# Optimization experiments

Hardware: AMD Instinct MI355X
Metric: run time of the kernel (lower is better)

## Reference

```python
import jax, jax.numpy as jnp
import numpy as np

K = 10          # number of neighbors (init kwarg k)
NUM_CLASSES = 100  # label vocabulary (targets drawn in [0, 100))


def setup_inputs() -> dict:
    key = jax.random.key(0)
    k1, k2, k3 = jax.random.split(key, 3)
    X = jax.random.normal(k1, (1024, 512), dtype=jnp.float32)
    data = jax.random.normal(k2, (50000, 512), dtype=jnp.float32)
    targets = jax.random.randint(k3, (50000,), 0, NUM_CLASSES, dtype=jnp.int64)
    return {"X": X, "data": data, "targets": targets}


def reference(X, data, targets):
    # Pairwise L2 distance (p=2 path of the module), computed via the
    x2 = jnp.sum(X * X, axis=1, keepdims=True)              # [Q, 1]
    d2 = jnp.sum(data * data, axis=1)                        # [N]
    sq = x2 + d2[None, :] - 2.0 * (X @ data.T)               # [Q, N]
    dist = jnp.sqrt(jnp.maximum(sq, 0.0))                    # torch.norm(p1-p2, p=2)

    # torch: sort distances ascending, take first k indices -> top-k smallest.
    _, idx = jax.lax.top_k(-dist, K)                         # [Q, K]
    labels = targets[idx]                                    # [Q, K]

    # torch.mode over the k neighbor labels: histogram + argmax.
    # argmax picks the first (smallest) class on ties, matching torch.mode.
    counts = jax.nn.one_hot(labels, NUM_CLASSES, dtype=jnp.float32).sum(axis=1)  # [Q, C]
    pred = jnp.argmax(counts, axis=1).astype(jnp.float32)    # [Q]
    return pred
```

## Files before the change

kernel.cpp:

```cpp
#include <hip/hip_runtime.h>
#include <math.h>
#include <limits.h>

#define QN 1024
#define NN 50000
#define NPAD 50048
#define DD 512
#define KNN 10
#define NT 128
#define QTB 128
#define BK 32
#define NS 391
#define QB 8
#define NSAMP 31
#define NREST (NS - NSAMP)
#define CAP 512

#define WS_D2  0
#define WS_TAU 50048
#define WS_CNT (WS_TAU + 2048)
#define WS_XH  (WS_CNT + 1024)
#define WS_XL  (WS_XH + QN * DD / 2)
#define WS_CKS (WS_XL + QN * DD / 2)
#define WS_BUF (WS_CKS + QN * NSAMP * KNN * 2)
#define WS_DH  (WS_BUF + QN * CAP * 2)
#define WS_DL  (WS_DH + NS * 16 * 2048)
#define WS_END (WS_DL + NS * 16 * 2048)

typedef __attribute__((ext_vector_type(8))) short short8;
typedef __attribute__((ext_vector_type(4))) float f32x4;
typedef unsigned long long u64;

__device__ __forceinline__ u64 mkkey(float f, int idx) {
  unsigned u = __float_as_uint(f);
  unsigned m = u ^ ((unsigned)((int)u >> 31) | 0x80000000u);
  return ((u64)m << 32) | (unsigned)idx;
}

__device__ __forceinline__ void cvt2(float x, float y, unsigned& hi, unsigned& lo) {
  unsigned ux = __float_as_uint(x), uy = __float_as_uint(y);
  unsigned rx = ux + 0x7fffu + ((ux >> 16) & 1u);
  unsigned ry = uy + 0x7fffu + ((uy >> 16) & 1u);
  hi = (rx >> 16) | (ry & 0xffff0000u);
  float xl = x - __uint_as_float(rx & 0xffff0000u);
  float yl = y - __uint_as_float(ry & 0xffff0000u);
  unsigned uxl = __float_as_uint(xl), uyl = __float_as_uint(yl);
  unsigned rxl = uxl + 0x7fffu + ((uxl >> 16) & 1u);
  unsigned ryl = uyl + 0x7fffu + ((uyl >> 16) & 1u);
  lo = (rxl >> 16) | (ryl & 0xffff0000u);
}

__device__ __forceinline__ void glds16(const void* g, void* l) {
  __builtin_amdgcn_global_load_lds(
      (const __attribute__((address_space(1))) unsigned*)g,
      (__attribute__((address_space(3))) unsigned*)l, 16, 0, 0);
}

__device__ __forceinline__ void ins10(u64* kl, u64 k) {
#pragma unroll
  for (int u = 0; u < KNN; u++) {
    u64 lo = (k < kl[u]) ? k : kl[u];
    u64 hi = (k < kl[u]) ? kl[u] : k;
    kl[u] = lo; k = hi;
  }
}

__global__ __launch_bounds__(256) void convx_kernel(
    const float* __restrict__ Xm, float* __restrict__ ws) {
  int w = threadIdx.x >> 6, lane = threadIdx.x & 63;
  int row = blockIdx.x * 4 + w;
  const float4* p = (const float4*)(Xm + (size_t)row * DD) + lane * 2;
  float4 v0 = p[0], v1 = p[1];
  unsigned h[4], l[4];
  cvt2(v0.x, v0.y, h[0], l[0]); cvt2(v0.z, v0.w, h[1], l[1]);
  cvt2(v1.x, v1.y, h[2], l[2]); cvt2(v1.z, v1.w, h[3], l[3]);
  ((uint4*)(ws + WS_XH))[row * 64 + lane] = make_uint4(h[0], h[1], h[2], h[3]);
  ((uint4*)(ws + WS_XL))[row * 64 + lane] = make_uint4(l[0], l[1], l[2], l[3]);
}

__global__ __launch_bounds__(256) void convd_kernel(
    const float* __restrict__ dat, float* __restrict__ ws) {
  const int slice = blockIdx.x;
  const int t = threadIdx.x;
  const int row = t >> 1, h2 = t & 1;
  const int gr = slice * NT + row;
  const int r15 = row & 15;
  float s = 0.f;
#pragma unroll
  for (int kc8 = 0; kc8 < 8; kc8++) {
    const int kc = h2 * 8 + kc8;
    float4 v[8];
    if (gr < NN) {
      const float4* src = (const float4*)(dat + (size_t)gr * DD + kc * 32);
#pragma unroll
      for (int j = 0; j < 8; j++) v[j] = src[j];
    } else {
#pragma unroll
      for (int j = 0; j < 8; j++) v[j] = make_float4(0.f, 0.f, 0.f, 0.f);
    }
    unsigned hw[16], lw[16];
#pragma unroll
    for (int j = 0; j < 8; j++) {
      s = fmaf(v[j].x, v[j].x, s); s = fmaf(v[j].y, v[j].y, s);
      s = fmaf(v[j].z, v[j].z, s); s = fmaf(v[j].w, v[j].w, s);
      cvt2(v[j].x, v[j].y, hw[2 * j], lw[2 * j]);
      cvt2(v[j].z, v[j].w, hw[2 * j + 1], lw[2 * j + 1]);
    }
    uint4* dhp = (uint4*)((unsigned char*)(ws + WS_DH) +
                          (((size_t)slice * 16 + kc) * 8 + (row >> 4)) * 1024);
    uint4* dlp = (uint4*)((unsigned char*)(ws + WS_DL) +
                          (((size_t)slice * 16 + kc) * 8 + (row >> 4)) * 1024);
#pragma unroll
    for (int qd = 0; qd < 4; qd++) {
      dhp[qd * 16 + r15] = make_uint4(hw[4 * qd], hw[4 * qd + 1], hw[4 * qd + 2], hw[4 * qd + 3]);
      dlp[qd * 16 + r15] = make_uint4(lw[4 * qd], lw[4 * qd + 1], lw[4 * qd + 2], lw[4 * qd + 3]);
    }
  }
  s += __shfl_xor(s, 1, 64);
  if (h2 == 0) ws[WS_D2 + gr] = (gr < NN) ? s : __builtin_inff();
}

struct StageT { unsigned char ah[8192], al[8192], bh[8192], bl[8192]; };
struct EpiT  { float sq[64][132]; };
struct ListT { u64 kl[64][4][KNN]; };
union SmemU { StageT s; EpiT e; ListT l; u64 tau[128]; };

template <int PRE, int MODE>
__global__ __launch_bounds__(256, 3) void knn_chunk(
    const float* __restrict__ dat, float* __restrict__ ws, int soff) {
  __shared__ __align__(16) SmemU sm;
  const int qbase = blockIdx.x * QTB;
  const int slice = blockIdx.y + soff;
  const int nbase = slice * NT;
  const int t = threadIdx.x;
  const int lane = t & 63, wave = t >> 6;
  const int wn = wave & 1, wq = wave >> 1;
  const unsigned short* xh = (const unsigned short*)(ws + WS_XH);
  const unsigned short* xl = (const unsigned short*)(ws + WS_XL);
  const unsigned char* dh = (const unsigned char*)(ws + WS_DH);
  const unsigned char* dl = (const unsigned char*)(ws + WS_DL);

  f32x4 acc[4][4];
#pragma unroll
  for (int i = 0; i < 4; i++)
#pragma unroll
    for (int j = 0; j < 4; j++) acc[i][j] = (f32x4)0.f;

  if (PRE) {
    auto stage = [&](int kc) {
#pragma unroll
      for (int i = 0; i < 4; i++) {
        int pp = wave * 4 + i;
        int p = pp & 7;
        const unsigned short* g = (pp < 8 ? xh : xl) +
            (size_t)(qbase + p * 16 + (lane & 15)) * DD + kc * 32 + (lane >> 4) * 8;
        glds16(g, (pp < 8 ? sm.s.ah : sm.s.al) + p * 1024);
      }
#pragma unroll
      for (int i = 0; i < 4; i++) {
        int pp = wave * 4 + i;
        int p = pp & 7;
        const unsigned char* g = (pp < 8 ? dh : dl) +
            (((size_t)slice * 16 + kc) * 8 + p) * 1024 + lane * 16;
        glds16(g, (pp < 8 ? sm.s.bh : sm.s.bl) + p * 1024);
      }
    };
    stage(0);
    for (int kc = 0; kc < 16; kc++) {
      __syncthreads();
      const int fragoff = lane * 16;
      short8 fah[4], fal[4], fbh[4], fbl[4];
#pragma unroll
      for (int i = 0; i < 4; i++) {
        fah[i] = *(const short8*)(sm.s.ah + (wq * 4 + i) * 1024 + fragoff);
        fal[i] = *(const short8*)(sm.s.al + (wq * 4 + i) * 1024 + fragoff);
        fbh[i] = *(const short8*)(sm.s.bh + (wn * 4 + i) * 1024 + fragoff);
        fbl[i] = *(const short8*)(sm.s.bl + (wn * 4 + i) * 1024 + fragoff);
      }
      __syncthreads();
      if (kc < 15) stage(kc + 1);
#pragma unroll
      for (int mt = 0; mt < 4; mt++)
#pragma unroll
        for (int nt = 0; nt < 4; nt++)
          acc[mt][nt] = __builtin_amdgcn_mfma_f32_16x16x32_bf16(fah[mt], fbh[nt], acc[mt][nt], 0, 0, 0);
#pragma unroll
      for (int mt = 0; mt < 4; mt++)
#pragma unroll
        for (int nt = 0; nt < 4; nt++)
          acc[mt][nt] = __builtin_amdgcn_mfma_f32_16x16x32_bf16(fah[mt], fbl[nt], acc[mt][nt], 0, 0, 0);
#pragma unroll
      for (int mt = 0; mt < 4; mt++)
#pragma unroll
        for (int nt = 0; nt < 4; nt++)
          acc[mt][nt] = __builtin_amdgcn_mfma_f32_16x16x32_bf16(fal[mt], fbh[nt], acc[mt][nt], 0, 0, 0);
    }
  } else {
    const int brow = t >> 1, bh_half = t & 1;
    const int bgr = nbase + brow;
    const int bpanel = (brow >> 4) * 1024;
    const int bchunk = (brow & 15) * 16;
    for (int kk = 0; kk < DD; kk += BK) {
      __syncthreads();
#pragma unroll
      for (int i = 0; i < 4; i++) {
        int pp = wave * 4 + i;
        int p = pp & 7;
        const unsigned short* g = (pp < 8 ? xh : xl) +
            (size_t)(qbase + p * 16 + (lane & 15)) * DD + kk + (lane >> 4) * 8;
        glds16(g, (pp < 8 ? sm.s.ah : sm.s.al) + p * 1024);
      }
      {
        float4 v0 = make_float4(0.f, 0.f, 0.f, 0.f), v1 = v0, v2 = v0, v3 = v0;
        if (bgr < NN) {
          const float4* src = (const float4*)(dat + (size_t)bgr * DD + kk + bh_half * 16);
          v0 = src[0]; v1 = src[1]; v2 = src[2]; v3 = src[3];
        }
        unsigned hw[8], lw[8];
        cvt2(v0.x, v0.y, hw[0], lw[0]); cvt2(v0.z, v0.w, hw[1], lw[1]);
        cvt2(v1.x, v1.y, hw[2], lw[2]); cvt2(v1.z, v1.w, hw[3], lw[3]);
        cvt2(v2.x, v2.y, hw[4], lw[4]); cvt2(v2.z, v2.w, hw[5], lw[5]);
        cvt2(v3.x, v3.y, hw[6], lw[6]); cvt2(v3.z, v3.w, hw[7], lw[7]);
        unsigned char* bhp = sm.s.bh + bpanel;
        unsigned char* blp = sm.s.bl + bpanel;
        *(uint4*)(bhp + (2 * bh_half) * 256 + bchunk)     = make_uint4(hw[0], hw[1], hw[2], hw[3]);
        *(uint4*)(bhp + (2 * bh_half + 1) * 256 + bchunk) = make_uint4(hw[4], hw[5], hw[6], hw[7]);
        *(uint4*)(blp + (2 * bh_half) * 256 + bchunk)     = make_uint4(lw[0], lw[1], lw[2], lw[3]);
        *(uint4*)(blp + (2 * bh_half + 1) * 256 + bchunk) = make_uint4(lw[4], lw[5], lw[6], lw[7]);
      }
      __syncthreads();
      const int fragoff = lane * 16;
      short8 fah[4], fal[4], fbh[4], fbl[4];
#pragma unroll
      for (int i = 0; i < 4; i++) {
        fah[i] = *(const short8*)(sm.s.ah + (wq * 4 + i) * 1024 + fragoff);
        fal[i] = *(const short8*)(sm.s.al + (wq * 4 + i) * 1024 + fragoff);
        fbh[i] = *(const short8*)(sm.s.bh + (wn * 4 + i) * 1024 + fragoff);
        fbl[i] = *(const short8*)(sm.s.bl + (wn * 4 + i) * 1024 + fragoff);
      }
#pragma unroll
      for (int mt = 0; mt < 4; mt++)
#pragma unroll
        for (int nt = 0; nt < 4; nt++) {
          acc[mt][nt] = __builtin_amdgcn_mfma_f32_16x16x32_bf16(fah[mt], fbh[nt], acc[mt][nt], 0, 0, 0);
          acc[mt][nt] = __builtin_amdgcn_mfma_f32_16x16x32_bf16(fah[mt], fbl[nt], acc[mt][nt], 0, 0, 0);
          acc[mt][nt] = __builtin_amdgcn_mfma_f32_16x16x32_bf16(fal[mt], fbh[nt], acc[mt][nt], 0, 0, 0);
        }
    }
  }

  if (MODE == 0) {
#pragma unroll
    for (int pass = 0; pass < 2; pass++) {
      __syncthreads();
      if (wq == pass) {
#pragma unroll
        for (int nt = 0; nt < 4; nt++) {
          int col = wn * 64 + nt * 16 + (lane & 15);
          float d2v = ws[WS_D2 + nbase + col];
#pragma unroll
          for (int mt = 0; mt < 4; mt++)
#pragma unroll
            for (int rg = 0; rg < 4; rg++) {
              int lr = mt * 16 + (lane >> 4) * 4 + rg;
              sm.e.sq[lr][col] = fmaf(-2.f, acc[mt][nt][rg], d2v);
            }
        }
      }
      __syncthreads();
      {
        const int r = t >> 2, s = t & 3;
        u64 kl[KNN];
#pragma unroll
        for (int u = 0; u < KNN; u++) kl[u] = ~0ull;
        for (int jj = 0; jj < 32; jj++) {
          int c = s * 32 + ((jj + r + 8 * s) & 31);
          float v = sm.e.sq[r][c];
          ins10(kl, mkkey(v, nbase + c));
        }
        __syncthreads();
#pragma unroll
        for (int u = 0; u < KNN; u++) sm.l.kl[r][s][u] = kl[u];
      }
      __syncthreads();
      if (t < 64) {
        u64* dst = ((u64*)(ws + WS_CKS)) +
                   ((size_t)(qbase + pass * 64 + t) * NSAMP + blockIdx.y) * KNN;
        int h0 = 0, h1 = 0, h2 = 0, h3 = 0;
        for (int pick = 0; pick < KNN; pick++) {
          u64 k0 = sm.l.kl[t][0][h0], k1 = sm.l.kl[t][1][h1];
          u64 k2 = sm.l.kl[t][2][h2], k3 = sm.l.kl[t][3][h3];
          u64 best = k0; int bm = 0;
          if (k1 < best) { best = k1; bm = 1; }
          if (k2 < best) { best = k2; bm = 2; }
          if (k3 < best) { best = k3; bm = 3; }
          dst[pick] = best;
          h0 += (bm == 0); h1 += (bm == 1); h2 += (bm == 2); h3 += (bm == 3);
        }
      }
    }
  } else {
    __syncthreads();
    if (t < 128) sm.tau[t] = ((const u64*)(ws + WS_TAU))[qbase + t];
    __syncthreads();
    unsigned* cnt = (unsigned*)(ws + WS_CNT);
    u64* buf = (u64*)(ws + WS_BUF);
    float d2v[4];
#pragma unroll
    for (int nt = 0; nt < 4; nt++)
      d2v[nt] = ws[WS_D2 + nbase + wn * 64 + nt * 16 + (lane & 15)];
#pragma unroll
    for (int mt = 0; mt < 4; mt++)
#pragma unroll
      for (int rg = 0; rg < 4; rg++) {
        int row = wq * 64 + mt * 16 + (lane >> 4) * 4 + rg;
        u64 tr = sm.tau[row];
#pragma unroll
        for (int nt = 0; nt < 4; nt++) {
          float d = fmaf(-2.f, acc[mt][nt][rg], d2v[nt]);
          int col = nbase + wn * 64 + nt * 16 + (lane & 15);
          u64 key = mkkey(d, col);
          if (key < tr) {
            int q = qbase + row;
            unsigned slot = atomicAdd(cnt + q, 1u);
            if (slot < CAP) buf[(size_t)q * CAP + slot] = key;
          }
        }
      }
  }
}

__global__ __launch_bounds__(64) void tau_kernel(float* __restrict__ ws) {
  const int q = blockIdx.x;
  const int t = threadIdx.x;
  const u64* samp = ((const u64*)(ws + WS_CKS)) + (size_t)q * NSAMP * KNN;
  const int NC = NSAMP * KNN;
  u64 kl[KNN];
#pragma unroll
  for (int u = 0; u < KNN; u++) kl[u] = ~0ull;
  for (int j = t; j < NC; j += 64) ins10(kl, samp[j]);
  __shared__ u64 wk[64][KNN];
  __shared__ u64 m2[8][KNN];
#pragma unroll
  for (int u = 0; u < KNN; u++) wk[t][u] = kl[u];
  __syncthreads();
  if (t < 8) {
    int h[8] = {0, 0, 0, 0, 0, 0, 0, 0};
    for (int pick = 0; pick < KNN; pick++) {
      u64 best = ~0ull; int bm = 0;
#pragma unroll
      for (int m = 0; m < 8; m++) {
        u64 km = wk[t * 8 + m][h[m]];
        if (km < best) { best = km; bm = m; }
      }
      m2[t][pick] = best;
#pragma unroll
      for (int m = 0; m < 8; m++) h[m] += (bm == m);
    }
  }
  __syncthreads();
  if (t == 0) {
    int h[8] = {0, 0, 0, 0, 0, 0, 0, 0};
    u64 best = 0;
    for (int pick = 0; pick < KNN; pick++) {
      best = ~0ull; int bm = 0;
#pragma unroll
      for (int m = 0; m < 8; m++) {
        u64 km = m2[m][h[m]];
        if (km < best) { best = km; bm = m; }
      }
#pragma unroll
      for (int m = 0; m < 8; m++) h[m] += (bm == m);
    }
    ((u64*)(ws + WS_TAU))[q] = best;
    ((unsigned*)(ws + WS_CNT))[q] = 0u;
  }
}

__global__ __launch_bounds__(64) void knn_final(
    const int* __restrict__ targets, float* __restrict__ ws,
    float* __restrict__ out) {
  const int q = blockIdx.x;
  const int t = threadIdx.x;
  const u64* samp = ((const u64*)(ws + WS_CKS)) + (size_t)q * NSAMP * KNN;
  const u64* buf = ((const u64*)(ws + WS_BUF)) + (size_t)q * CAP;
  unsigned c = ((const unsigned*)(ws + WS_CNT))[q];
  if (c > CAP) c = CAP;

  u64 kl[KNN];
#pragma unroll
  for (int u = 0; u < KNN; u++) kl[u] = ~0ull;
  for (int j = t; j < NSAMP * KNN; j += 64) ins10(kl, samp[j]);
  for (int j = t; j < (int)c; j += 64) ins10(kl, buf[j]);

  __shared__ u64 wk[64][KNN];
  __shared__ u64 m2[8][KNN];
#pragma unroll
  for (int u = 0; u < KNN; u++) wk[t][u] = kl[u];
  __syncthreads();
  if (t < 8) {
    int h[8] = {0, 0, 0, 0, 0, 0, 0, 0};
    for (int pick = 0; pick < KNN; pick++) {
      u64 best = ~0ull; int bm = 0;
#pragma unroll
      for (int m = 0; m < 8; m++) {
        u64 km = wk[t * 8 + m][h[m]];
        if (km < best) { best = km; bm = m; }
      }
      m2[t][pick] = best;
#pragma unroll
      for (int m = 0; m < 8; m++) h[m] += (bm == m);
    }
  }
  __syncthreads();
  if (t == 0) {
    int h[8] = {0, 0, 0, 0, 0, 0, 0, 0};
    int fi[KNN];
    for (int pick = 0; pick < KNN; pick++) {
      u64 best = ~0ull; int bm = 0;
#pragma unroll
      for (int m = 0; m < 8; m++) {
        u64 km = m2[m][h[m]];
        if (km < best) { best = km; bm = m; }
      }
      fi[pick] = (int)(unsigned)(best & 0xffffffffu);
#pragma unroll
      for (int m = 0; m < 8; m++) h[m] += (bm == m);
    }
    int lab[KNN];
#pragma unroll
    for (int u = 0; u < KNN; u++) lab[u] = targets[fi[u]];
    int bc = 0, bl = INT_MAX;
#pragma unroll
    for (int i = 0; i < KNN; i++) {
      int cc = 0;
#pragma unroll
      for (int j = 0; j < KNN; j++) cc += (lab[j] == lab[i]) ? 1 : 0;
      if (cc > bc || (cc == bc && lab[i] < bl)) { bc = cc; bl = lab[i]; }
    }
    out[q] = (float)bl;
  }
}

extern "C" void kernel_launch(void* const* d_in, const int* in_sizes, int n_in,
                              void* d_out, int out_size, void* d_ws, size_t ws_size,
                              hipStream_t stream) {
  const float* Xm  = (const float*)d_in[0];
  const float* dat = (const float*)d_in[1];
  const int* targets = (const int*)d_in[2];
  float* out = (float*)d_out;
  float* ws  = (float*)d_ws;
  const bool pre = ws_size >= (size_t)WS_END * 4;

  hipLaunchKernelGGL(convx_kernel, dim3(QN / 4), dim3(256), 0, stream, Xm, ws);
  hipLaunchKernelGGL(convd_kernel, dim3(NS), dim3(256), 0, stream, dat, ws);
  if (pre) {
    hipLaunchKernelGGL((knn_chunk<1, 0>), dim3(QB, NSAMP), dim3(256), 0, stream, dat, ws, 0);
    hipLaunchKernelGGL(tau_kernel, dim3(QN), dim3(64), 0, stream, ws);
    hipLaunchKernelGGL((knn_chunk<1, 1>), dim3(QB, NREST), dim3(256), 0, stream, dat, ws, NSAMP);
  } else {
    hipLaunchKernelGGL((knn_chunk<0, 0>), dim3(QB, NSAMP), dim3(256), 0, stream, dat, ws, 0);
    hipLaunchKernelGGL(tau_kernel, dim3(QN), dim3(64), 0, stream, ws);
    hipLaunchKernelGGL((knn_chunk<0, 1>), dim3(QB, NREST), dim3(256), 0, stream, dat, ws, NSAMP);
  }
  hipLaunchKernelGGL(knn_final, dim3(QN), dim3(64), 0, stream, targets, ws, out);
}
```

Before: 387.4 us.

## Shrink MODE-1 shared memory, raise occupancy hint, and swizzle block order for L2 reuse

Specializes the shared-memory union per MODE, so the MODE-1 pass only reserves the 32 KB staging buffers instead of the larger epilogue and list arrays. It raises the launch-bounds minimum blocks per CU from 3 to 5. For MODE 1 it remaps block indices so that groups of eight consecutive blocks cover different data slices across query tiles, aiming for better L2 locality. The higher occupancy target may force the compiler to spill registers given the large 4x4 MFMA accumulator array, and it also applies to MODE 0, whose shared footprint is unchanged.

```diff
diff --git a/kernel.cpp b/kernel.cpp
--- a/kernel.cpp
+++ b/kernel.cpp
@@ -123,14 +123,26 @@
 struct StageT { unsigned char ah[8192], al[8192], bh[8192], bl[8192]; };
 struct EpiT  { float sq[64][132]; };
 struct ListT { u64 kl[64][4][KNN]; };
-union SmemU { StageT s; EpiT e; ListT l; u64 tau[128]; };
+
+template <int MODE> union SmemU { StageT s; EpiT e; ListT l; };
+template <> union SmemU<1> { StageT s; };
 
 template <int PRE, int MODE>
-__global__ __launch_bounds__(256, 3) void knn_chunk(
+__global__ __launch_bounds__(256, 5) void knn_chunk(
     const float* __restrict__ dat, float* __restrict__ ws, int soff) {
-  __shared__ __align__(16) SmemU sm;
-  const int qbase = blockIdx.x * QTB;
-  const int slice = blockIdx.y + soff;
+  __shared__ __align__(16) SmemU<MODE> sm;
+  int bqx, bsy;
+  if (MODE == 1 && (gridDim.y & 7) == 0) {
+    const int n = (int)(blockIdx.y * gridDim.x + blockIdx.x);
+    const int m = n >> 3;
+    const int ypx = (int)(gridDim.y >> 3);
+    bqx = m & 7;
+    bsy = (n & 7) * ypx + (m >> 3);
+  } else {
+    bqx = blockIdx.x; bsy = blockIdx.y;
+  }
+  const int qbase = bqx * QTB;
+  const int slice = bsy + soff;
   const int nbase = slice * NT;
   const int t = threadIdx.x;
   const int lane = t & 63, wave = t >> 6;
@@ -250,6 +262,7 @@
   }
 
   if (MODE == 0) {
+    SmemU<0>* smp = (SmemU<0>*)&sm;
 #pragma unroll
     for (int pass = 0; pass < 2; pass++) {
       __syncthreads();
@@ -263,7 +276,7 @@
 #pragma unroll
             for (int rg = 0; rg < 4; rg++) {
               int lr = mt * 16 + (lane >> 4) * 4 + rg;
-              sm.e.sq[lr][col] = fmaf(-2.f, acc[mt][nt][rg], d2v);
+              smp->e.sq[lr][col] = fmaf(-2.f, acc[mt][nt][rg], d2v);
             }
         }
       }
@@ -275,12 +288,12 @@
         for (int u = 0; u < KNN; u++) kl[u] = ~0ull;
         for (int jj = 0; jj < 32; jj++) {
           int c = s * 32 + ((jj + r + 8 * s) & 31);
-          float v = sm.e.sq[r][c];
+          float v = smp->e.sq[r][c];
           ins10(kl, mkkey(v, nbase + c));
         }
         __syncthreads();
 #pragma unroll
-        for (int u = 0; u < KNN; u++) sm.l.kl[r][s][u] = kl[u];
+        for (int u = 0; u < KNN; u++) smp->l.kl[r][s][u] = kl[u];
       }
       __syncthreads();
       if (t < 64) {
@@ -288,8 +301,8 @@
                    ((size_t)(qbase + pass * 64 + t) * NSAMP + blockIdx.y) * KNN;
         int h0 = 0, h1 = 0, h2 = 0, h3 = 0;
         for (int pick = 0; pick < KNN; pick++) {
-          u64 k0 = sm.l.kl[t][0][h0], k1 = sm.l.kl[t][1][h1];
-          u64 k2 = sm.l.kl[t][2][h2], k3 = sm.l.kl[t][3][h3];
+          u64 k0 = smp->l.kl[t][0][h0], k1 = smp->l.kl[t][1][h1];
+          u64 k2 = smp->l.kl[t][2][h2], k3 = smp->l.kl[t][3][h3];
           u64 best = k0; int bm = 0;
           if (k1 < best) { best = k1; bm = 1; }
           if (k2 < best) { best = k2; bm = 2; }
@@ -301,7 +314,8 @@
     }
   } else {
     __syncthreads();
-    if (t < 128) sm.tau[t] = ((const u64*)(ws + WS_TAU))[qbase + t];
+    u64* taub = (u64*)&sm;
+    if (t < 128) taub[t] = ((const u64*)(ws + WS_TAU))[qbase + t];
     __syncthreads();
     unsigned* cnt = (unsigned*)(ws + WS_CNT);
     u64* buf = (u64*)(ws + WS_BUF);
@@ -314,7 +328,7 @@
 #pragma unroll
       for (int rg = 0; rg < 4; rg++) {
         int row = wq * 64 + mt * 16 + (lane >> 4) * 4 + rg;
-        u64 tr = sm.tau[row];
+        u64 tr = taub[row];
 #pragma unroll
         for (int nt = 0; nt < 4; nt++) {
           float d = fmaf(-2.f, acc[mt][nt][rg], d2v[nt]);
```

New measurement: 735.3 us. +89.8%, slower.

## Pre-swizzle X into MFMA fragment layout and load A fragments directly from global

Applied to the files above, without the earlier changes.

convx now writes the bf16 hi/lo query matrix in MFMA fragment order, so the GEMM kernel loads A fragments straight from global/L2 into registers instead of staging them through LDS. That halves shared memory per block, which can raise occupancy, and removes the A-side LDS traffic. In return each wave issues more global loads. The MODE 1 kernel also remaps block indices so blocks that run together share query tiles across slices, aiming for better cache locality. Trade-off: A loads are no longer prefetched a stage ahead, so their latency may be exposed.

```diff
diff --git a/kernel.cpp b/kernel.cpp
--- a/kernel.cpp
+++ b/kernel.cpp
@@ -67,15 +67,17 @@
 
 __global__ __launch_bounds__(256) void convx_kernel(
     const float* __restrict__ Xm, float* __restrict__ ws) {
-  int w = threadIdx.x >> 6, lane = threadIdx.x & 63;
-  int row = blockIdx.x * 4 + w;
-  const float4* p = (const float4*)(Xm + (size_t)row * DD) + lane * 2;
+  const int g = blockIdx.x * 256 + threadIdx.x;
+  const int b = g >> 10, kc = (g >> 6) & 15, l = g & 63;
+  const int row = b * 16 + (l & 15);
+  const int col = kc * 32 + (l >> 4) * 8;
+  const float4* p = (const float4*)(Xm + (size_t)row * DD + col);
   float4 v0 = p[0], v1 = p[1];
-  unsigned h[4], l[4];
-  cvt2(v0.x, v0.y, h[0], l[0]); cvt2(v0.z, v0.w, h[1], l[1]);
-  cvt2(v1.x, v1.y, h[2], l[2]); cvt2(v1.z, v1.w, h[3], l[3]);
-  ((uint4*)(ws + WS_XH))[row * 64 + lane] = make_uint4(h[0], h[1], h[2], h[3]);
-  ((uint4*)(ws + WS_XL))[row * 64 + lane] = make_uint4(l[0], l[1], l[2], l[3]);
+  unsigned h[4], lo[4];
+  cvt2(v0.x, v0.y, h[0], lo[0]); cvt2(v0.z, v0.w, h[1], lo[1]);
+  cvt2(v1.x, v1.y, h[2], lo[2]); cvt2(v1.z, v1.w, h[3], lo[3]);
+  ((uint4*)(ws + WS_XH))[g] = make_uint4(h[0], h[1], h[2], h[3]);
+  ((uint4*)(ws + WS_XL))[g] = make_uint4(lo[0], lo[1], lo[2], lo[3]);
 }
 
 __global__ __launch_bounds__(256) void convd_kernel(
@@ -120,25 +122,42 @@
   if (h2 == 0) ws[WS_D2 + gr] = (gr < NN) ? s : __builtin_inff();
 }
 
-struct StageT { unsigned char ah[8192], al[8192], bh[8192], bl[8192]; };
+struct StageT { unsigned char bh[8192], bl[8192]; };
 struct EpiT  { float sq[64][132]; };
 struct ListT { u64 kl[64][4][KNN]; };
-union SmemU { StageT s; EpiT e; ListT l; u64 tau[128]; };
+
+template <int MODE> struct SmemSel {
+  union U { StageT s; EpiT e; ListT l; };
+};
+template <> struct SmemSel<1> {
+  struct U { StageT s; u64 tau[128]; };
+};
 
 template <int PRE, int MODE>
 __global__ __launch_bounds__(256, 3) void knn_chunk(
     const float* __restrict__ dat, float* __restrict__ ws, int soff) {
-  __shared__ __align__(16) SmemU sm;
-  const int qbase = blockIdx.x * QTB;
-  const int slice = blockIdx.y + soff;
+  __shared__ __align__(16) typename SmemSel<MODE>::U sm;
+  int bqx, bsy;
+  if (MODE == 1 && (gridDim.y & 7) == 0) {
+    const int n = (int)(blockIdx.y * gridDim.x + blockIdx.x);
+    const int m = n >> 3;
+    const int ypx = (int)(gridDim.y >> 3);
+    bqx = m & 7;
+    bsy = (n & 7) * ypx + (m >> 3);
+  } else {
+    bqx = blockIdx.x; bsy = blockIdx.y;
+  }
+  const int qbase = bqx * QTB;
+  const int slice = bsy + soff;
   const int nbase = slice * NT;
   const int t = threadIdx.x;
   const int lane = t & 63, wave = t >> 6;
   const int wn = wave & 1, wq = wave >> 1;
-  const unsigned short* xh = (const unsigned short*)(ws + WS_XH);
-  const unsigned short* xl = (const unsigned short*)(ws + WS_XL);
   const unsigned char* dh = (const unsigned char*)(ws + WS_DH);
   const unsigned char* dl = (const unsigned char*)(ws + WS_DL);
+  const char* xfh = (const char*)(ws + WS_XH);
+  const char* xfl = (const char*)(ws + WS_XL);
+  const int abase = (((bqx * 8 + wq * 4) * 16) * 64 + lane) * 16;
 
   f32x4 acc[4][4];
 #pragma unroll
@@ -146,39 +165,37 @@
 #pragma unroll
     for (int j = 0; j < 4; j++) acc[i][j] = (f32x4)0.f;
 
+  auto stageB = [&](int kc) {
+#pragma unroll
+    for (int i = 0; i < 4; i++) {
+      int pp = wave * 4 + i;
+      int p = pp & 7;
+      const unsigned char* g = (pp < 8 ? dh : dl) +
+          (((size_t)slice * 16 + kc) * 8 + p) * 1024 + lane * 16;
+      glds16(g, (pp < 8 ? sm.s.bh : sm.s.bl) + p * 1024);
+    }
+  };
+
   if (PRE) {
-    auto stage = [&](int kc) {
+    stageB(0);
+    for (int kc = 0; kc < 16; kc++) {
+      short8 fah[4], fal[4];
 #pragma unroll
       for (int i = 0; i < 4; i++) {
-        int pp = wave * 4 + i;
-        int p = pp & 7;
-        const unsigned short* g = (pp < 8 ? xh : xl) +
-            (size_t)(qbase + p * 16 + (lane & 15)) * DD + kc * 32 + (lane >> 4) * 8;
-        glds16(g, (pp < 8 ? sm.s.ah : sm.s.al) + p * 1024);
-      }
+        int off = abase + (i * 1024 + kc * 64) * 16;
+        fah[i] = *(const short8*)(xfh + off);
+        fal[i] = *(const short8*)(xfl + off);
+      }
+      __syncthreads();
+      const int fragoff = lane * 16;
+      short8 fbh[4], fbl[4];
 #pragma unroll
       for (int i = 0; i < 4; i++) {
-        int pp = wave * 4 + i;
-        int p = pp & 7;
-        const unsigned char* g = (pp < 8 ? dh : dl) +
-            (((size_t)slice * 16 + kc) * 8 + p) * 1024 + lane * 16;
-        glds16(g, (pp < 8 ? sm.s.bh : sm.s.bl) + p * 1024);
-      }
-    };
-    stage(0);
-    for (int kc = 0; kc < 16; kc++) {
-      __syncthreads();
-      const int fragoff = lane * 16;
-      short8 fah[4], fal[4], fbh[4], fbl[4];
-#pragma unroll
-      for (int i = 0; i < 4; i++) {
-        fah[i] = *(const short8*)(sm.s.ah + (wq * 4 + i) * 1024 + fragoff);
-        fal[i] = *(const short8*)(sm.s.al + (wq * 4 + i) * 1024 + fragoff);
         fbh[i] = *(const short8*)(sm.s.bh + (wn * 4 + i) * 1024 + fragoff);
         fbl[i] = *(const short8*)(sm.s.bl + (wn * 4 + i) * 1024 + fragoff);
       }
       __syncthreads();
-      if (kc < 15) stage(kc + 1);
+      if (kc < 15) stageB(kc + 1);
 #pragma unroll
       for (int mt = 0; mt < 4; mt++)
 #pragma unroll
@@ -200,16 +217,16 @@
     const int bgr = nbase + brow;
     const int bpanel = (brow >> 4) * 1024;
     const int bchunk = (brow & 15) * 16;
-    for (int kk = 0; kk < DD; kk += BK) {
-      __syncthreads();
+    for (int kc = 0; kc < 16; kc++) {
+      const int kk = kc * BK;
+      short8 fah[4], fal[4];
 #pragma unroll
       for (int i = 0; i < 4; i++) {
-        int pp = wave * 4 + i;
-        int p = pp & 7;
-        const unsigned short* g = (pp < 8 ? xh : xl) +
-            (size_t)(qbase + p * 16 + (lane & 15)) * DD + kk + (lane >> 4) * 8;
-        glds16(g, (pp < 8 ? sm.s.ah : sm.s.al) + p * 1024);
-      }
+        int off = abase + (i * 1024 + kc * 64) * 16;
+        fah[i] = *(const short8*)(xfh + off);
+        fal[i] = *(const short8*)(xfl + off);
+      }
+      __syncthreads();
       {
         float4 v0 = make_float4(0.f, 0.f, 0.f, 0.f), v1 = v0, v2 = v0, v3 = v0;
         if (bgr < NN) {
@@ -230,14 +247,13 @@
       }
       __syncthreads();
       const int fragoff = lane * 16;
-      short8 fah[4], fal[4], fbh[4], fbl[4];
+      short8 fbh[4], fbl[4];
 #pragma unroll
       for (int i = 0; i < 4; i++) {
-        fah[i] = *(const short8*)(sm.s.ah + (wq * 4 + i) * 1024 + fragoff);
-        fal[i] = *(const short8*)(sm.s.al + (wq * 4 + i) * 1024 + fragoff);
         fbh[i] = *(const short8*)(sm.s.bh + (wn * 4 + i) * 1024 + fragoff);
         fbl[i] = *(const short8*)(sm.s.bl + (wn * 4 + i) * 1024 + fragoff);
       }
+      __syncthreads();
 #pragma unroll
       for (int mt = 0; mt < 4; mt++)
 #pragma unroll
@@ -249,7 +265,7 @@
     }
   }
 
-  if (MODE == 0) {
+  if constexpr (MODE == 0) {
 #pragma unroll
     for (int pass = 0; pass < 2; pass++) {
       __syncthreads();
@@ -300,7 +316,6 @@
       }
     }
   } else {
-    __syncthreads();
     if (t < 128) sm.tau[t] = ((const u64*)(ws + WS_TAU))[qbase + t];
     __syncthreads();
     unsigned* cnt = (unsigned*)(ws + WS_CNT);
@@ -452,7 +467,7 @@
   float* ws  = (float*)d_ws;
   const bool pre = ws_size >= (size_t)WS_END * 4;
 
-  hipLaunchKernelGGL(convx_kernel, dim3(QN / 4), dim3(256), 0, stream, Xm, ws);
+  hipLaunchKernelGGL(convx_kernel, dim3(QN * DD / 8 / 256), dim3(256), 0, stream, Xm, ws);
   hipLaunchKernelGGL(convd_kernel, dim3(NS), dim3(256), 0, stream, dat, ws);
   if (pre) {
     hipLaunchKernelGGL((knn_chunk<1, 0>), dim3(QB, NSAMP), dim3(256), 0, stream, dat, ws, 0);
```

Result: faster. 363.9 us (-6.1%).
